# Kernel optimization log

Measured on AMD Instinct MI355X. Metric: run time of the kernel, lower is better.

## Reference

```python
import jax, jax.numpy as jnp
import numpy as np

T, A, E, D, INTER = 2048, 2, 8, 2048, 4096


def setup_inputs() -> dict:
    key = jax.random.key(0)
    k_x, k_idx, k1, k2, k3 = jax.random.split(key, 5)
    scale = 0.02
    return {
        "x": jax.random.normal(k_x, (T, D), dtype=jnp.float32),
        "expert_indices": jax.random.randint(k_idx, (T, A), 0, E, dtype=jnp.int32),
        "w1": jax.random.normal(k1, (E, INTER, D), dtype=jnp.float32) * scale,
        "w2": jax.random.normal(k2, (E, D, INTER), dtype=jnp.float32) * scale,
        "w3": jax.random.normal(k3, (E, INTER, D), dtype=jnp.float32) * scale,
    }


def reference(x, expert_indices, w1, w2, w3):
    # Mathematically identical to out[t,a] = silu(w1[e] @ x[t]) * (w3[e] @ x[t]) @ w2[e].T
    # with e = expert_indices[t,a]. We compute all experts densely (batched GEMMs)
    # and gather per-token expert outputs, avoiding the (T,A,Inter,D) weight blowup.
    x1 = jax.nn.silu(jnp.einsum('td,eod->teo', x, w1))   # (T,E,Inter)
    x3 = jnp.einsum('td,eod->teo', x, w3)                # (T,E,Inter)
    out_all = jnp.einsum('teo,edo->ted', x1 * x3, w2)    # (T,E,D)
    # gather expert outputs per token: (T,A,D)
    return jnp.take_along_axis(out_all, expert_indices[:, :, None], axis=1)
```

## Files before the change

### kernel.cpp

```cpp
#include <hip/hip_runtime.h>
#include <hip/hip_bf16.h>


#define T_TOK 2048
#define A_ACT 2
#define E_EXP 8
#define D_DIM 2048
#define I_DIM 4096
#define TA    (T_TOK * A_ACT)
#define BK    32

typedef __attribute__((ext_vector_type(4))) float f32x4;
typedef __attribute__((ext_vector_type(8))) short bf16x8;

static __device__ __forceinline__ short f2bf(float f) {
  union { __hip_bfloat16 b; short s; } u;
  u.b = __float2bfloat16(f);
  return u.s;
}

static __device__ __forceinline__ void gload_lds16(const void* g, void* l) {
  __builtin_amdgcn_global_load_lds(
      (const __attribute__((address_space(1))) unsigned int*)g,
      (__attribute__((address_space(3))) unsigned int*)l, 16, 0, 0);
}

__global__ void route_kernel(const int* __restrict__ idx, int* __restrict__ off,
                             int* __restrict__ perm) {
  __shared__ int scnt[E_EXP];
  __shared__ int scur[E_EXP];
  __shared__ int soff[E_EXP + 1];
  const int t = threadIdx.x;
  if (t < E_EXP) scnt[t] = 0;
  __syncthreads();
  for (int i = t; i < TA; i += 1024) atomicAdd(&scnt[idx[i]], 1);
  __syncthreads();
  if (t == 0) {
    int s = 0;
    for (int e = 0; e < E_EXP; ++e) { soff[e] = s; s += scnt[e]; }
    soff[E_EXP] = s;
  }
  __syncthreads();
  if (t < E_EXP) scur[t] = soff[t];
  if (t <= E_EXP) off[t] = soff[t];
  __syncthreads();
  for (int i = t; i < TA; i += 1024) {
    int e = idx[i];
    int p = atomicAdd(&scur[e], 1);
    perm[p] = i;
  }
}

__global__ void gather_x(const float* __restrict__ x, const int* __restrict__ perm,
                         short* __restrict__ xg) {
  const int r = blockIdx.x;
  const int tok = perm[r] / A_ACT;
  const f32x4* src = (const f32x4*)(x + (size_t)tok * D_DIM);
  const int c = threadIdx.x;
  f32x4 v0 = src[c * 2 + 0];
  f32x4 v1 = src[c * 2 + 1];
  bf16x8 o;
#pragma unroll
  for (int j = 0; j < 4; ++j) { o[j] = f2bf(v0[j]); o[4 + j] = f2bf(v1[j]); }
  *(bf16x8*)(xg + (size_t)r * D_DIM + c * 8) = o;
}


__global__ __launch_bounds__(512, 2)
void gemm1_w13(const short* __restrict__ xg, const float* __restrict__ w1,
               const float* __restrict__ w3, const int* __restrict__ off,
               short* __restrict__ h) {
  const int e = blockIdx.z;
  const int off_e = off[e];
  const int cnt = off[e + 1] - off_e;
  const int n0 = blockIdx.y * 1024;
  if (n0 >= cnt) return;
  const int m0 = blockIdx.x * 32;

  __shared__ __align__(16) short sA[2][1024 * BK];
  __shared__ __align__(16) short sB1[2][32 * BK];
  __shared__ __align__(16) short sB3[2][32 * BK];

  const int tid = threadIdx.x;
  const int w = tid >> 6;
  const int lane = tid & 63;
  const int lr = lane & 15;
  const int kq = lane >> 4;
  const int pq = kq ^ ((lr >> 1) & 3);
  const bool wactive = (w * 128 < cnt - n0);

  const short* gA[8];
#pragma unroll
  for (int j = 0; j < 8; ++j) {
    int seg = (w * 8 + j) * 64 + lane;
    int row = seg >> 2;
    int qp = seg & 3;
    int ql = qp ^ ((row >> 1) & 3);
    int trow = n0 + row; if (trow > cnt - 1) trow = cnt - 1;
    gA[j] = xg + (size_t)(off_e + trow) * D_DIM + ql * 8;
  }
  const bool bstage = (tid < 256);
  const int bts = tid & 127;
  const int bwr = bts >> 2;
  const int bqp = bts & 3;
  const float* gB;
  {
    int ql = bqp ^ ((bwr >> 1) & 3);
    const float* wsel = (tid < 128) ? w1 : w3;
    gB = wsel + (size_t)e * I_DIM * D_DIM + (size_t)(m0 + bwr) * D_DIM + ql * 8;
  }

  f32x4 acc1[8][2], acc3[8][2];
#pragma unroll
  for (int mi = 0; mi < 8; ++mi)
#pragma unroll
    for (int ni = 0; ni < 2; ++ni) {
      acc1[mi][ni] = (f32x4){0.f, 0.f, 0.f, 0.f};
      acc3[mi][ni] = (f32x4){0.f, 0.f, 0.f, 0.f};
    }

  auto stageA = [&](int nb, int k0) {
#pragma unroll
    for (int j = 0; j < 8; ++j)
      gload_lds16(gA[j] + k0, &sA[nb][(w * 8 + j) * 512]);
  };
  auto loadB = [&](int k0, f32x4& ra, f32x4& rb) {
    if (bstage) {
      const float* p = gB + k0;
      ra = *(const f32x4*)p;
      rb = *(const f32x4*)(p + 4);
    }
  };
  auto writeB = [&](int nb, const f32x4& ra, const f32x4& rb) {
    if (bstage) {
      bf16x8 o;
#pragma unroll
      for (int j = 0; j < 4; ++j) { o[j] = f2bf(ra[j]); o[4 + j] = f2bf(rb[j]); }
      short* dst = ((tid < 128) ? sB1[nb] : sB3[nb]) + bwr * BK + bqp * 8;
      *(bf16x8*)dst = o;
    }
  };

  const int NSTEP = D_DIM / BK;
  {
    f32x4 ra, rb;
    if (wactive) stageA(0, 0);
    loadB(0, ra, rb);
    writeB(0, ra, rb);
    __syncthreads();
  }
  for (int t = 0; t < NSTEP; ++t) {
    const int nb = t & 1, pf = nb ^ 1;
    const bool pfv = (t + 1 < NSTEP);
    f32x4 ra, rb;
    if (pfv) {
      if (wactive) stageA(pf, (t + 1) * BK);
      loadB((t + 1) * BK, ra, rb);
    }
    if (wactive) {
      const short* Ab = sA[nb] + ((w * 128 + lr) * BK + pq * 8);
      bf16x8 af[8];
#pragma unroll
      for (int mi = 0; mi < 8; ++mi)
        af[mi] = *(const bf16x8*)(Ab + mi * 16 * BK);
#pragma unroll
      for (int ni = 0; ni < 2; ++ni) {
        const int brow = ni * 16 + lr;
        bf16x8 b1 = *(const bf16x8*)(sB1[nb] + brow * BK + pq * 8);
        bf16x8 b3 = *(const bf16x8*)(sB3[nb] + brow * BK + pq * 8);
#pragma unroll
        for (int mi = 0; mi < 8; ++mi) {
          acc1[mi][ni] = __builtin_amdgcn_mfma_f32_16x16x32_bf16(af[mi], b1, acc1[mi][ni], 0, 0, 0);
          acc3[mi][ni] = __builtin_amdgcn_mfma_f32_16x16x32_bf16(af[mi], b3, acc3[mi][ni], 0, 0, 0);
        }
      }
    }
    if (pfv) writeB(pf, ra, rb);
    __syncthreads();
  }

  if (wactive) {
#pragma unroll
    for (int mi = 0; mi < 8; ++mi)
#pragma unroll
      for (int ni = 0; ni < 2; ++ni)
#pragma unroll
        for (int j = 0; j < 4; ++j) {
          int row = w * 128 + mi * 16 + kq * 4 + j;
          if (n0 + row < cnt) {
            int col = m0 + ni * 16 + lr;
            float z1 = acc1[mi][ni][j];
            float z3 = acc3[mi][ni][j];
            float sv = z1 / (1.0f + __expf(-z1));
            h[(size_t)(off_e + n0 + row) * I_DIM + col] = f2bf(sv * z3);
          }
        }
  }
}

__global__ __launch_bounds__(512, 2)
void gemm2_out(const short* __restrict__ h, const float* __restrict__ w2,
               const int* __restrict__ off, const int* __restrict__ perm,
               float* __restrict__ out) {
  const int e = blockIdx.z;
  const int off_e = off[e];
  const int cnt = off[e + 1] - off_e;
  const int n0 = blockIdx.y * 1024;
  if (n0 >= cnt) return;
  const int d0 = blockIdx.x * 64;

  __shared__ __align__(16) short sA[2][1024 * BK];
  __shared__ __align__(16) short sB[2][64 * BK];

  const int tid = threadIdx.x;
  const int w = tid >> 6;
  const int lane = tid & 63;
  const int lr = lane & 15;
  const int kq = lane >> 4;
  const int pq = kq ^ ((lr >> 1) & 3);
  const bool wactive = (w * 128 < cnt - n0);

  const short* gA[8];
#pragma unroll
  for (int j = 0; j < 8; ++j) {
    int seg = (w * 8 + j) * 64 + lane;
    int row = seg >> 2;
    int qp = seg & 3;
    int ql = qp ^ ((row >> 1) & 3);
    int trow = n0 + row; if (trow > cnt - 1) trow = cnt - 1;
    gA[j] = h + (size_t)(off_e + trow) * I_DIM + ql * 8;
  }
  const bool bstage = (tid < 256);
  const int bwr = (tid & 255) >> 2;
  const int bqp = tid & 3;
  const float* gB;
  {
    int ql = bqp ^ ((bwr >> 1) & 3);
    gB = w2 + (size_t)e * D_DIM * I_DIM + (size_t)(d0 + bwr) * I_DIM + ql * 8;
  }

  f32x4 acc[8][4];
#pragma unroll
  for (int mi = 0; mi < 8; ++mi)
#pragma unroll
    for (int ni = 0; ni < 4; ++ni) acc[mi][ni] = (f32x4){0.f, 0.f, 0.f, 0.f};

  auto stageA = [&](int nb, int k0) {
#pragma unroll
    for (int j = 0; j < 8; ++j)
      gload_lds16(gA[j] + k0, &sA[nb][(w * 8 + j) * 512]);
  };
  auto loadB = [&](int k0, f32x4& ra, f32x4& rb) {
    if (bstage) {
      const float* p = gB + k0;
      ra = *(const f32x4*)p;
      rb = *(const f32x4*)(p + 4);
    }
  };
  auto writeB = [&](int nb, const f32x4& ra, const f32x4& rb) {
    if (bstage) {
      bf16x8 o;
#pragma unroll
      for (int j = 0; j < 4; ++j) { o[j] = f2bf(ra[j]); o[4 + j] = f2bf(rb[j]); }
      *(bf16x8*)(sB[nb] + bwr * BK + bqp * 8) = o;
    }
  };

  const int NSTEP = I_DIM / BK;
  {
    f32x4 ra, rb;
    if (wactive) stageA(0, 0);
    loadB(0, ra, rb);
    writeB(0, ra, rb);
    __syncthreads();
  }
  for (int t = 0; t < NSTEP; ++t) {
    const int nb = t & 1, pf = nb ^ 1;
    const bool pfv = (t + 1 < NSTEP);
    f32x4 ra, rb;
    if (pfv) {
      if (wactive) stageA(pf, (t + 1) * BK);
      loadB((t + 1) * BK, ra, rb);
    }
    if (wactive) {
      const short* Ab = sA[nb] + ((w * 128 + lr) * BK + pq * 8);
      bf16x8 af[8];
#pragma unroll
      for (int mi = 0; mi < 8; ++mi)
        af[mi] = *(const bf16x8*)(Ab + mi * 16 * BK);
#pragma unroll
      for (int ni = 0; ni < 4; ++ni) {
        bf16x8 b = *(const bf16x8*)(sB[nb] + (ni * 16 + lr) * BK + pq * 8);
#pragma unroll
        for (int mi = 0; mi < 8; ++mi)
          acc[mi][ni] = __builtin_amdgcn_mfma_f32_16x16x32_bf16(af[mi], b, acc[mi][ni], 0, 0, 0);
      }
    }
    if (pfv) writeB(pf, ra, rb);
    __syncthreads();
  }

  if (wactive) {
#pragma unroll
    for (int mi = 0; mi < 8; ++mi)
#pragma unroll
      for (int j = 0; j < 4; ++j) {
        int row = w * 128 + mi * 16 + kq * 4 + j;
        if (n0 + row < cnt) {
          int oi = perm[off_e + n0 + row];
#pragma unroll
          for (int ni = 0; ni < 4; ++ni)
            out[(size_t)oi * D_DIM + d0 + ni * 16 + lr] = acc[mi][ni][j];
        }
      }
  }
}

extern "C" void kernel_launch(void* const* d_in, const int* in_sizes, int n_in,
                              void* d_out, int out_size, void* d_ws, size_t ws_size,
                              hipStream_t stream) {
  const float* x  = (const float*)d_in[0];
  const int* idx  = (const int*)d_in[1];
  const float* w1 = (const float*)d_in[2];
  const float* w2 = (const float*)d_in[3];
  const float* w3 = (const float*)d_in[4];
  float* out = (float*)d_out;

  int* off  = (int*)d_ws;
  int* perm = off + 16;
  short* xg = (short*)((char*)d_ws + 32768);
  short* h  = (short*)((char*)d_ws + 32768 + (size_t)16 * 1024 * 1024);

  route_kernel<<<1, 1024, 0, stream>>>(idx, off, perm);
  gather_x<<<TA, 256, 0, stream>>>(x, perm, xg);
  gemm1_w13<<<dim3(I_DIM / 32, TA / 1024, E_EXP), 512, 0, stream>>>(xg, w1, w3, off, h);
  gemm2_out<<<dim3(D_DIM / 64, TA / 1024, E_EXP), 512, 0, stream>>>(h, w2, off, perm, out);
}
```

Before: 1.154 ms.

## Retile MoE GEMMs to 256-token tiles with 2D warp layout and higher occupancy

Both expert GEMMs shrink the token tile from 1024 to 256 rows. Waves are arranged as a 4x2 grid, so each wave computes a 64x32 sub-tile. gemm1 widens its weight tile from 32 to 64 columns, and launch bounds rise to 4 blocks per CU. The goal is less work wasted on padded token rows per expert, more blocks to balance across CUs, and smaller per-wave accumulators. In exchange, each weight tile is reused by fewer tokens, so fp32 weights are reloaded and converted more often. Inactive waves now also issue A-tile loads.

```diff
diff --git a/kernel.cpp b/kernel.cpp
--- a/kernel.cpp
+++ b/kernel.cpp
@@ -66,20 +66,20 @@
 }
 
 
-__global__ __launch_bounds__(512, 2)
+__global__ __launch_bounds__(512, 4)
 void gemm1_w13(const short* __restrict__ xg, const float* __restrict__ w1,
                const float* __restrict__ w3, const int* __restrict__ off,
                short* __restrict__ h) {
   const int e = blockIdx.z;
   const int off_e = off[e];
   const int cnt = off[e + 1] - off_e;
-  const int n0 = blockIdx.y * 1024;
+  const int n0 = blockIdx.y * 256;
   if (n0 >= cnt) return;
-  const int m0 = blockIdx.x * 32;
-
-  __shared__ __align__(16) short sA[2][1024 * BK];
-  __shared__ __align__(16) short sB1[2][32 * BK];
-  __shared__ __align__(16) short sB3[2][32 * BK];
+  const int m0 = blockIdx.x * 64;
+
+  __shared__ __align__(16) short sA[2][256 * BK];
+  __shared__ __align__(16) short sB1[2][64 * BK];
+  __shared__ __align__(16) short sB3[2][64 * BK];
 
   const int tid = threadIdx.x;
   const int w = tid >> 6;
@@ -87,32 +87,34 @@
   const int lr = lane & 15;
   const int kq = lane >> 4;
   const int pq = kq ^ ((lr >> 1) & 3);
-  const bool wactive = (w * 128 < cnt - n0);
-
-  const short* gA[8];
-#pragma unroll
-  for (int j = 0; j < 8; ++j) {
-    int seg = (w * 8 + j) * 64 + lane;
-    int row = seg >> 2;
-    int qp = seg & 3;
+  const int wt = w >> 1;
+  const int wi = w & 1;
+  const bool wactive = (wt * 64 < cnt - n0);
+
+  const short* gA[2];
+#pragma unroll
+  for (int j = 0; j < 2; ++j) {
+    int seg = w * 2 + j;
+    int q = seg * 64 + lane;
+    int row = q >> 2;
+    int qp = q & 3;
     int ql = qp ^ ((row >> 1) & 3);
     int trow = n0 + row; if (trow > cnt - 1) trow = cnt - 1;
     gA[j] = xg + (size_t)(off_e + trow) * D_DIM + ql * 8;
   }
-  const bool bstage = (tid < 256);
-  const int bts = tid & 127;
+  const int bts = tid & 255;
   const int bwr = bts >> 2;
   const int bqp = bts & 3;
   const float* gB;
   {
     int ql = bqp ^ ((bwr >> 1) & 3);
-    const float* wsel = (tid < 128) ? w1 : w3;
+    const float* wsel = (tid < 256) ? w1 : w3;
     gB = wsel + (size_t)e * I_DIM * D_DIM + (size_t)(m0 + bwr) * D_DIM + ql * 8;
   }
 
-  f32x4 acc1[8][2], acc3[8][2];
-#pragma unroll
-  for (int mi = 0; mi < 8; ++mi)
+  f32x4 acc1[4][2], acc3[4][2];
+#pragma unroll
+  for (int mi = 0; mi < 4; ++mi)
 #pragma unroll
     for (int ni = 0; ni < 2; ++ni) {
       acc1[mi][ni] = (f32x4){0.f, 0.f, 0.f, 0.f};
@@ -121,30 +123,26 @@
 
   auto stageA = [&](int nb, int k0) {
 #pragma unroll
-    for (int j = 0; j < 8; ++j)
-      gload_lds16(gA[j] + k0, &sA[nb][(w * 8 + j) * 512]);
+    for (int j = 0; j < 2; ++j)
+      gload_lds16(gA[j] + k0, &sA[nb][(w * 2 + j) * 512]);
   };
   auto loadB = [&](int k0, f32x4& ra, f32x4& rb) {
-    if (bstage) {
-      const float* p = gB + k0;
-      ra = *(const f32x4*)p;
-      rb = *(const f32x4*)(p + 4);
-    }
+    const float* p = gB + k0;
+    ra = *(const f32x4*)p;
+    rb = *(const f32x4*)(p + 4);
   };
   auto writeB = [&](int nb, const f32x4& ra, const f32x4& rb) {
-    if (bstage) {
-      bf16x8 o;
-#pragma unroll
-      for (int j = 0; j < 4; ++j) { o[j] = f2bf(ra[j]); o[4 + j] = f2bf(rb[j]); }
-      short* dst = ((tid < 128) ? sB1[nb] : sB3[nb]) + bwr * BK + bqp * 8;
-      *(bf16x8*)dst = o;
-    }
+    bf16x8 o;
+#pragma unroll
+    for (int j = 0; j < 4; ++j) { o[j] = f2bf(ra[j]); o[4 + j] = f2bf(rb[j]); }
+    short* dst = ((tid < 256) ? sB1[nb] : sB3[nb]) + bwr * BK + bqp * 8;
+    *(bf16x8*)dst = o;
   };
 
   const int NSTEP = D_DIM / BK;
   {
     f32x4 ra, rb;
-    if (wactive) stageA(0, 0);
+    stageA(0, 0);
     loadB(0, ra, rb);
     writeB(0, ra, rb);
     __syncthreads();
@@ -154,22 +152,22 @@
     const bool pfv = (t + 1 < NSTEP);
     f32x4 ra, rb;
     if (pfv) {
-      if (wactive) stageA(pf, (t + 1) * BK);
+      stageA(pf, (t + 1) * BK);
       loadB((t + 1) * BK, ra, rb);
     }
     if (wactive) {
-      const short* Ab = sA[nb] + ((w * 128 + lr) * BK + pq * 8);
-      bf16x8 af[8];
-#pragma unroll
-      for (int mi = 0; mi < 8; ++mi)
+      const short* Ab = sA[nb] + ((wt * 64 + lr) * BK + pq * 8);
+      bf16x8 af[4];
+#pragma unroll
+      for (int mi = 0; mi < 4; ++mi)
         af[mi] = *(const bf16x8*)(Ab + mi * 16 * BK);
 #pragma unroll
       for (int ni = 0; ni < 2; ++ni) {
-        const int brow = ni * 16 + lr;
+        const int brow = wi * 32 + ni * 16 + lr;
         bf16x8 b1 = *(const bf16x8*)(sB1[nb] + brow * BK + pq * 8);
         bf16x8 b3 = *(const bf16x8*)(sB3[nb] + brow * BK + pq * 8);
 #pragma unroll
-        for (int mi = 0; mi < 8; ++mi) {
+        for (int mi = 0; mi < 4; ++mi) {
           acc1[mi][ni] = __builtin_amdgcn_mfma_f32_16x16x32_bf16(af[mi], b1, acc1[mi][ni], 0, 0, 0);
           acc3[mi][ni] = __builtin_amdgcn_mfma_f32_16x16x32_bf16(af[mi], b3, acc3[mi][ni], 0, 0, 0);
         }
@@ -181,14 +179,14 @@
 
   if (wactive) {
 #pragma unroll
-    for (int mi = 0; mi < 8; ++mi)
+    for (int mi = 0; mi < 4; ++mi)
 #pragma unroll
       for (int ni = 0; ni < 2; ++ni)
 #pragma unroll
         for (int j = 0; j < 4; ++j) {
-          int row = w * 128 + mi * 16 + kq * 4 + j;
+          int row = wt * 64 + mi * 16 + kq * 4 + j;
           if (n0 + row < cnt) {
-            int col = m0 + ni * 16 + lr;
+            int col = m0 + wi * 32 + ni * 16 + lr;
             float z1 = acc1[mi][ni][j];
             float z3 = acc3[mi][ni][j];
             float sv = z1 / (1.0f + __expf(-z1));
@@ -198,18 +196,18 @@
   }
 }
 
-__global__ __launch_bounds__(512, 2)
+__global__ __launch_bounds__(512, 4)
 void gemm2_out(const short* __restrict__ h, const float* __restrict__ w2,
                const int* __restrict__ off, const int* __restrict__ perm,
                float* __restrict__ out) {
   const int e = blockIdx.z;
   const int off_e = off[e];
   const int cnt = off[e + 1] - off_e;
-  const int n0 = blockIdx.y * 1024;
+  const int n0 = blockIdx.y * 256;
   if (n0 >= cnt) return;
   const int d0 = blockIdx.x * 64;
 
-  __shared__ __align__(16) short sA[2][1024 * BK];
+  __shared__ __align__(16) short sA[2][256 * BK];
   __shared__ __align__(16) short sB[2][64 * BK];
 
   const int tid = threadIdx.x;
@@ -218,14 +216,17 @@
   const int lr = lane & 15;
   const int kq = lane >> 4;
   const int pq = kq ^ ((lr >> 1) & 3);
-  const bool wactive = (w * 128 < cnt - n0);
-
-  const short* gA[8];
-#pragma unroll
-  for (int j = 0; j < 8; ++j) {
-    int seg = (w * 8 + j) * 64 + lane;
-    int row = seg >> 2;
-    int qp = seg & 3;
+  const int wt = w >> 1;
+  const int wi = w & 1;
+  const bool wactive = (wt * 64 < cnt - n0);
+
+  const short* gA[2];
+#pragma unroll
+  for (int j = 0; j < 2; ++j) {
+    int seg = w * 2 + j;
+    int q = seg * 64 + lane;
+    int row = q >> 2;
+    int qp = q & 3;
     int ql = qp ^ ((row >> 1) & 3);
     int trow = n0 + row; if (trow > cnt - 1) trow = cnt - 1;
     gA[j] = h + (size_t)(off_e + trow) * I_DIM + ql * 8;
@@ -239,16 +240,16 @@
     gB = w2 + (size_t)e * D_DIM * I_DIM + (size_t)(d0 + bwr) * I_DIM + ql * 8;
   }
 
-  f32x4 acc[8][4];
-#pragma unroll
-  for (int mi = 0; mi < 8; ++mi)
-#pragma unroll
-    for (int ni = 0; ni < 4; ++ni) acc[mi][ni] = (f32x4){0.f, 0.f, 0.f, 0.f};
+  f32x4 acc[4][2];
+#pragma unroll
+  for (int mi = 0; mi < 4; ++mi)
+#pragma unroll
+    for (int ni = 0; ni < 2; ++ni) acc[mi][ni] = (f32x4){0.f, 0.f, 0.f, 0.f};
 
   auto stageA = [&](int nb, int k0) {
 #pragma unroll
-    for (int j = 0; j < 8; ++j)
-      gload_lds16(gA[j] + k0, &sA[nb][(w * 8 + j) * 512]);
+    for (int j = 0; j < 2; ++j)
+      gload_lds16(gA[j] + k0, &sA[nb][(w * 2 + j) * 512]);
   };
   auto loadB = [&](int k0, f32x4& ra, f32x4& rb) {
     if (bstage) {
@@ -269,7 +270,7 @@
   const int NSTEP = I_DIM / BK;
   {
     f32x4 ra, rb;
-    if (wactive) stageA(0, 0);
+    stageA(0, 0);
     loadB(0, ra, rb);
     writeB(0, ra, rb);
     __syncthreads();
@@ -279,20 +280,21 @@
     const bool pfv = (t + 1 < NSTEP);
     f32x4 ra, rb;
     if (pfv) {
-      if (wactive) stageA(pf, (t + 1) * BK);
+      stageA(pf, (t + 1) * BK);
       loadB((t + 1) * BK, ra, rb);
     }
     if (wactive) {
-      const short* Ab = sA[nb] + ((w * 128 + lr) * BK + pq * 8);
-      bf16x8 af[8];
-#pragma unroll
-      for (int mi = 0; mi < 8; ++mi)
+      const short* Ab = sA[nb] + ((wt * 64 + lr) * BK + pq * 8);
+      bf16x8 af[4];
+#pragma unroll
+      for (int mi = 0; mi < 4; ++mi)
         af[mi] = *(const bf16x8*)(Ab + mi * 16 * BK);
 #pragma unroll
-      for (int ni = 0; ni < 4; ++ni) {
-        bf16x8 b = *(const bf16x8*)(sB[nb] + (ni * 16 + lr) * BK + pq * 8);
-#pragma unroll
-        for (int mi = 0; mi < 8; ++mi)
+      for (int ni = 0; ni < 2; ++ni) {
+        const int brow = wi * 32 + ni * 16 + lr;
+        bf16x8 b = *(const bf16x8*)(sB[nb] + brow * BK + pq * 8);
+#pragma unroll
+        for (int mi = 0; mi < 4; ++mi)
           acc[mi][ni] = __builtin_amdgcn_mfma_f32_16x16x32_bf16(af[mi], b, acc[mi][ni], 0, 0, 0);
       }
     }
@@ -302,15 +304,15 @@
 
   if (wactive) {
 #pragma unroll
-    for (int mi = 0; mi < 8; ++mi)
+    for (int mi = 0; mi < 4; ++mi)
 #pragma unroll
       for (int j = 0; j < 4; ++j) {
-        int row = w * 128 + mi * 16 + kq * 4 + j;
+        int row = wt * 64 + mi * 16 + kq * 4 + j;
         if (n0 + row < cnt) {
           int oi = perm[off_e + n0 + row];
 #pragma unroll
-          for (int ni = 0; ni < 4; ++ni)
-            out[(size_t)oi * D_DIM + d0 + ni * 16 + lr] = acc[mi][ni][j];
+          for (int ni = 0; ni < 2; ++ni)
+            out[(size_t)oi * D_DIM + d0 + wi * 32 + ni * 16 + lr] = acc[mi][ni][j];
         }
       }
   }
@@ -333,6 +335,6 @@
 
   route_kernel<<<1, 1024, 0, stream>>>(idx, off, perm);
   gather_x<<<TA, 256, 0, stream>>>(x, perm, xg);
-  gemm1_w13<<<dim3(I_DIM / 32, TA / 1024, E_EXP), 512, 0, stream>>>(xg, w1, w3, off, h);
-  gemm2_out<<<dim3(D_DIM / 64, TA / 1024, E_EXP), 512, 0, stream>>>(h, w2, off, perm, out);
-}
+  gemm1_w13<<<dim3(I_DIM / 64, TA / 256, E_EXP), 512, 0, stream>>>(xg, w1, w3, off, h);
+  gemm2_out<<<dim3(D_DIM / 64, TA / 256, E_EXP), 512, 0, stream>>>(h, w2, off, perm, out);
+}
```

New measurement: 1.001 ms. 1.15x faster.
